# Optimization experiments

Hardware: AMD Instinct MI355X
Metric: run time of the kernel (lower is better)

Reference implementation:

```python
import jax, jax.numpy as jnp
import numpy as np

HID = 2048          # hidden_size
INTER = 4096        # expand * hidden_size
NH = 64             # num_heads
HD = 64             # head_dim (NH*HD == INTER)
N = 128             # ssm state_size
G = 1               # n_groups
K = 4               # conv_kernel
EPS = 1e-5
CONV_DIM = INTER + 2 * G * N            # 4352
PROJ = INTER + CONV_DIM + NH            # 8512 (d_mlp == 0)


def setup_inputs() -> dict:
    key = jax.random.key(0)
    ks = jax.random.split(key, 6)
    B, S = 2, 2048
    return {
        "hidden_states": jax.random.normal(ks[0], (B, S, HID), jnp.float32),
        "in_proj_w": jax.random.normal(ks[1], (PROJ, HID), jnp.float32) * 0.02,
        "conv_w": jax.random.normal(ks[2], (CONV_DIM, 1, K), jnp.float32) * 0.1,
        "conv_b": jax.random.normal(ks[3], (CONV_DIM,), jnp.float32) * 0.02,
        "dt_bias": jnp.ones((NH,), jnp.float32),
        "A_log": jnp.log(jnp.arange(1, NH + 1, dtype=jnp.float32)),
        "D": jnp.ones((NH,), jnp.float32),
        "norm_weight": jnp.ones((INTER,), jnp.float32),
        "out_proj_w": jax.random.normal(ks[4], (HID, INTER), jnp.float32) * 0.02,
    }


def _mamba2_forward(hidden_states, in_proj_w, conv_w, conv_b, dt_bias,
                    A_log, D, norm_weight, out_proj_w):
    b, sq, _ = hidden_states.shape
    # in_proj (d_mlp == 0, so split is gate | hidden_B_C | dt)
    proj = hidden_states @ in_proj_w.T                       # [b, s, PROJ]
    gate, hbc, dt = jnp.split(proj, [INTER, INTER + CONV_DIM], axis=-1)

    # causal depthwise conv1d over time + SiLU
    xc = jnp.transpose(hbc, (0, 2, 1))                       # [b, conv_dim, s]
    xc = jax.lax.conv_general_dilated(xc, conv_w, (1,), [(K - 1, 0)],
                                      feature_group_count=CONV_DIM)
    xc = xc + conv_b[None, :, None]
    hbc = jax.nn.silu(jnp.transpose(xc, (0, 2, 1)))          # [b, s, conv_dim]

    hs, Bm, Cm = jnp.split(hbc, [INTER, INTER + G * N], axis=-1)
    hs = hs.reshape(b, sq, NH, HD)
    Bm = jnp.repeat(Bm.reshape(b, sq, G, N), NH // G, axis=2)   # [b, s, nh, n]
    Cm = jnp.repeat(Cm.reshape(b, sq, G, N), NH // G, axis=2)

    A = -jnp.exp(A_log)                                      # [nh]
    dt = jax.nn.softplus(dt + dt_bias)                       # [b, s, nh]

    # selective SSM scan: state_t = exp(dt*A)*state_{t-1} + dt*B_t x_t^T
    def step(state, inp):
        xt, Bt, Ct, dtt = inp                                # [b,nh,hd],[b,nh,n],[b,nh,n],[b,nh]
        dA = jnp.exp(dtt * A)                                # [b, nh]
        state = state * dA[..., None, None] \
            + (dtt[..., None] * xt)[..., None] * Bt[:, :, None, :]
        y = jnp.einsum('bhdn,bhn->bhd', state, Ct)
        return state, y

    init = jnp.zeros((b, NH, HD, N), jnp.float32)
    xs = (jnp.moveaxis(hs, 1, 0), jnp.moveaxis(Bm, 1, 0),
          jnp.moveaxis(Cm, 1, 0), jnp.moveaxis(dt, 1, 0))
    _, ys = jax.lax.scan(step, init, xs)                     # [s, b, nh, hd]
    y = jnp.moveaxis(ys, 0, 1) + D[None, None, :, None] * hs
    y = y.reshape(b, sq, INTER)

    # gated RMSNorm (norm_before_gate=False): gate first, then normalize
    y = y * jax.nn.silu(gate)
    var = jnp.mean(y * y, axis=-1, keepdims=True)
    y = y * jax.lax.rsqrt(var + EPS) * norm_weight
    return y @ out_proj_w.T                                  # [b, s, HID]


def reference(hidden_states, in_proj_w, conv_w, conv_b, dt_bias, A_log, D,
              norm_weight, out_proj_w):
    return _mamba2_forward(hidden_states, in_proj_w, conv_w, conv_b, dt_bias,
                           A_log, D, norm_weight, out_proj_w)
```

## Files before the change

kernel.cpp:

```cpp
#include <hip/hip_runtime.h>
#include <hip/hip_bf16.h>
#include <cstddef>
#include <cstdint>

#define HID   2048
#define INTER 4096
#define NH    64
#define HD    64
#define NST   128
#define CONV_DIM 4352
#define PROJ  8512
#define PROJ_PAD 8704
#define SS    2048
#define BB    2
#define BS    (BB*SS)
#define EPS   1e-5f

#define COL_HS 4096
#define COL_B  8192
#define COL_C  8320
#define COL_DT 8448

#define NCH   16
#define CHUNK 128

#define CL    128
#define NCHK  16

typedef short s16x8 __attribute__((ext_vector_type(8)));
typedef float f32x4 __attribute__((ext_vector_type(4)));

__device__ inline ushort f2b(float x) {
  __hip_bfloat16 h = __float2bfloat16(x);
  return *(ushort*)&h;
}
__device__ inline float b2f(ushort u) {
  unsigned int v = ((unsigned int)u) << 16;
  return __uint_as_float(v);
}
__device__ inline int swz(int row, int e) { return row * 128 + (e ^ ((row & 7) << 3)); }

__device__ inline void gload16(const void* g, void* l) {
  __builtin_amdgcn_global_load_lds((const __attribute__((address_space(1))) void*)g,
                                   (__attribute__((address_space(3))) void*)l, 16, 0, 0);
}

__global__ __launch_bounds__(256) void to_bf16(const float* __restrict__ src,
                                               ushort* __restrict__ dst, long n4) {
  long i = (long)blockIdx.x * 256 + threadIdx.x;
  if (i >= n4) return;
  float4 v = *(const float4*)(src + i * 4);
  ushort4 o;
  o.x = f2b(v.x); o.y = f2b(v.y); o.z = f2b(v.z); o.w = f2b(v.w);
  *(ushort4*)(dst + i * 4) = o;
}

__global__ __launch_bounds__(256) void to_bf16_pad(const float* __restrict__ src,
                                                   ushort* __restrict__ dst, long n4) {
  long i = (long)blockIdx.x * 256 + threadIdx.x;
  if (i >= n4) return;
  long e0 = i * 4;
  long row = e0 >> 11;
  ushort4 o;
  if (row < PROJ) {
    float4 v = *(const float4*)(src + e0);
    o.x = f2b(v.x); o.y = f2b(v.y); o.z = f2b(v.z); o.w = f2b(v.w);
  } else {
    o.x = o.y = o.z = o.w = 0;
  }
  *(ushort4*)(dst + e0) = o;
}

__global__ __launch_bounds__(512, 2) void gemm256_8ph(
    const ushort* __restrict__ A, const ushort* __restrict__ Bw,
    float* __restrict__ C) {
  __shared__ ushort smem[65536];
  const int tid = threadIdx.x;
  const int lane = tid & 63;
  const int wid = tid >> 6;
  const int wm = wid >> 2;
  const int wn = wid & 3;
  const int r = lane & 15;
  const int kx = lane >> 4;

  const int fid = blockIdx.x;
  const int bcol = ((fid >> 7) << 3) + ((fid & 127) >> 4);
  const int brow = fid & 15;

  const ushort* Ag = A + (size_t)(brow * 256) * HID;
  const ushort* Bg = Bw + (size_t)(bcol * 256) * HID;

  const int srow = tid >> 3;
  const int scole = (((tid & 7) * 16) ^ ((srow & 7) << 4)) >> 1;

  auto stageA = [&](int buf, int kt, int half) {
    const ushort* g = Ag + (size_t)(half * 128 + srow) * HID + kt * 64 + scole;
    ushort* l = smem + buf * 16384 + half * 8192 + tid * 8;
    gload16(g, l);
    gload16(g + (size_t)64 * HID, l + 4096);
  };
  auto stageB = [&](int buf, int kt, int half) {
    const ushort* g = Bg + (size_t)(half * 128 + srow) * HID + kt * 64 + scole;
    ushort* l = smem + 32768 + buf * 16384 + half * 8192 + tid * 8;
    gload16(g, l);
    gload16(g + (size_t)64 * HID, l + 4096);
  };
  auto ldA = [&](int buf, int mf, int ks) -> s16x8 {
    int row = wm * 128 + mf * 16 + r;
    int cb = (ks * 64 + kx * 16) ^ ((row & 7) << 4);
    return *(const s16x8*)(smem + buf * 16384 + row * 64 + (cb >> 1));
  };
  auto ldB = [&](int buf, int nf, int ks) -> s16x8 {
    int row = wn * 64 + nf * 16 + r;
    int cb = (ks * 64 + kx * 16) ^ ((row & 7) << 4);
    return *(const s16x8*)(smem + 32768 + buf * 16384 + row * 64 + (cb >> 1));
  };

  f32x4 acc[8][4];
#pragma unroll
  for (int i = 0; i < 8; i++)
#pragma unroll
    for (int j = 0; j < 4; j++) acc[i][j] = (f32x4)0.f;

  constexpr int NT = HID / 64;

  stageA(0, 0, 0); stageA(0, 0, 1);
  stageB(0, 0, 0); stageB(0, 0, 1);
  stageA(1, 1, 0); stageA(1, 1, 1);
  asm volatile("s_waitcnt vmcnt(4)" ::: "memory");
  __builtin_amdgcn_s_barrier();

  int cur = 0;
  for (int t = 0; t < NT; t++) {
    s16x8 a[4][2], b[2][2], b2[2][2];
#pragma unroll
    for (int mf = 0; mf < 4; mf++)
#pragma unroll
      for (int ks = 0; ks < 2; ks++) a[mf][ks] = ldA(cur, mf, ks);
#pragma unroll
    for (int nf = 0; nf < 2; nf++)
#pragma unroll
      for (int ks = 0; ks < 2; ks++) b[nf][ks] = ldB(cur, nf, ks);
    if (t + 1 < NT) stageB(cur ^ 1, t + 1, 0);
    __builtin_amdgcn_s_barrier();
    asm volatile("s_waitcnt lgkmcnt(0)" ::: "memory");
    __builtin_amdgcn_sched_barrier(0);
    __builtin_amdgcn_s_setprio(1);
#pragma unroll
    for (int mf = 0; mf < 4; mf++)
#pragma unroll
      for (int nf = 0; nf < 2; nf++)
#pragma unroll
        for (int ks = 0; ks < 2; ks++)
          acc[mf][nf] = __builtin_amdgcn_mfma_f32_16x16x32_bf16(a[mf][ks], b[nf][ks], acc[mf][nf], 0, 0, 0);
    __builtin_amdgcn_s_setprio(0);
    __builtin_amdgcn_s_barrier();
#pragma unroll
    for (int nf = 0; nf < 2; nf++)
#pragma unroll
      for (int ks = 0; ks < 2; ks++) b2[nf][ks] = ldB(cur, nf + 2, ks);
    if (t + 1 < NT) stageB(cur ^ 1, t + 1, 1);
    __builtin_amdgcn_s_barrier();
    asm volatile("s_waitcnt lgkmcnt(0)" ::: "memory");
    __builtin_amdgcn_sched_barrier(0);
    __builtin_amdgcn_s_setprio(1);
#pragma unroll
    for (int mf = 0; mf < 4; mf++)
#pragma unroll
      for (int nf = 0; nf < 2; nf++)
#pragma unroll
        for (int ks = 0; ks < 2; ks++)
          acc[mf][nf + 2] = __builtin_amdgcn_mfma_f32_16x16x32_bf16(a[mf][ks], b2[nf][ks], acc[mf][nf + 2], 0, 0, 0);
    __builtin_amdgcn_s_setprio(0);
    __builtin_amdgcn_s_barrier();
#pragma unroll
    for (int mf = 0; mf < 4; mf++)
#pragma unroll
      for (int ks = 0; ks < 2; ks++) a[mf][ks] = ldA(cur, mf + 4, ks);
    __builtin_amdgcn_s_barrier();
    asm volatile("s_waitcnt lgkmcnt(0)" ::: "memory");
    __builtin_amdgcn_sched_barrier(0);
    __builtin_amdgcn_s_setprio(1);
#pragma unroll
    for (int mf = 0; mf < 4; mf++)
#pragma unroll
      for (int nf = 0; nf < 2; nf++)
#pragma unroll
        for (int ks = 0; ks < 2; ks++)
          acc[mf + 4][nf] = __builtin_amdgcn_mfma_f32_16x16x32_bf16(a[mf][ks], b[nf][ks], acc[mf + 4][nf], 0, 0, 0);
    __builtin_amdgcn_s_setprio(0);
    __builtin_amdgcn_s_barrier();
    if (t + 2 < NT) { stageA(cur, t + 2, 0); stageA(cur, t + 2, 1); }
    __builtin_amdgcn_s_setprio(1);
#pragma unroll
    for (int mf = 0; mf < 4; mf++)
#pragma unroll
      for (int nf = 0; nf < 2; nf++)
#pragma unroll
        for (int ks = 0; ks < 2; ks++)
          acc[mf + 4][nf + 2] = __builtin_amdgcn_mfma_f32_16x16x32_bf16(a[mf][ks], b2[nf][ks], acc[mf + 4][nf + 2], 0, 0, 0);
    __builtin_amdgcn_s_setprio(0);
    if (t + 2 < NT) {
      asm volatile("s_waitcnt vmcnt(4)" ::: "memory");
    } else {
      asm volatile("s_waitcnt vmcnt(0)" ::: "memory");
    }
    __builtin_amdgcn_s_barrier();
    cur ^= 1;
  }

  const int m0 = brow * 256 + wm * 128 + (lane >> 4) * 4;
  const int n0 = bcol * 256 + wn * 64 + r;
#pragma unroll
  for (int mf = 0; mf < 8; mf++) {
#pragma unroll
    for (int nf = 0; nf < 4; nf++) {
      int n = n0 + nf * 16;
      if (n >= PROJ) continue;
#pragma unroll
      for (int q = 0; q < 4; q++)
        C[(size_t)(m0 + mf * 16 + q) * PROJ + n] = acc[mf][nf][q];
    }
  }
}

template <bool GUARD_N>
__global__ __launch_bounds__(256) void gemm_bt16(
    const ushort* __restrict__ A, int lda,
    const ushort* __restrict__ Bw, int ldb,
    float* __restrict__ C, int ldc, int Kd, int Nmax) {
  __shared__ short smem[8192];
  const int tid = threadIdx.x;
  const int lane = tid & 63;
  const int wid = tid >> 6;
  const int wm = wid >> 1, wn = wid & 1;
  const int r = lane & 15;
  const int kx = lane >> 4;

  const int fid = blockIdx.y * gridDim.x + blockIdx.x;
  const int bcol = ((fid >> 8) << 3) | ((fid & 255) >> 5);
  const int brow = fid & 31;

  const ushort* Ab = A + (size_t)(brow * 128) * lda;
  const ushort* Bb = Bw + (size_t)(bcol * 128) * ldb;

  f32x4 acc[4][4];
#pragma unroll
  for (int i = 0; i < 4; i++)
#pragma unroll
    for (int j = 0; j < 4; j++) acc[i][j] = (f32x4)0.f;

  const int u0 = tid, u1 = 256 + tid;
  const int row0 = u0 >> 2, kc0 = (u0 & 3) * 8;
  const int row1 = u1 >> 2, kc1 = (u1 & 3) * 8;

  const s16x8* As8 = (const s16x8*)smem;
  const s16x8* Bs8 = (const s16x8*)(smem + 4096);

  for (int k0 = 0; k0 < Kd; k0 += 32) {
    __syncthreads();
    gload16(Ab + (size_t)row0 * lda + k0 + kc0, smem + u0 * 8);
    gload16(Ab + (size_t)row1 * lda + k0 + kc1, smem + u1 * 8);
    gload16(Bb + (size_t)row0 * ldb + k0 + kc0, smem + 4096 + u0 * 8);
    gload16(Bb + (size_t)row1 * ldb + k0 + kc1, smem + 4096 + u1 * 8);
    __syncthreads();
    s16x8 af[4], bw[4];
#pragma unroll
    for (int i = 0; i < 4; i++) af[i] = As8[(wm * 64 + i * 16 + r) * 4 + kx];
#pragma unroll
    for (int j = 0; j < 4; j++) bw[j] = Bs8[(wn * 64 + j * 16 + r) * 4 + kx];
#pragma unroll
    for (int i = 0; i < 4; i++)
#pragma unroll
      for (int j = 0; j < 4; j++)
        acc[i][j] = __builtin_amdgcn_mfma_f32_16x16x32_bf16(af[i], bw[j], acc[i][j], 0, 0, 0);
  }

  const int m0 = brow * 128 + wm * 64 + (lane >> 4) * 4;
  const int n0 = bcol * 128 + wn * 64 + (lane & 15);
#pragma unroll
  for (int i = 0; i < 4; i++) {
#pragma unroll
    for (int j = 0; j < 4; j++) {
      int n = n0 + j * 16;
      if (GUARD_N && n >= Nmax) continue;
#pragma unroll
      for (int q = 0; q < 4; q++) {
        C[(size_t)(m0 + i * 16 + q) * ldc + n] = acc[i][j][q];
      }
    }
  }
}

__global__ void conv_capture(const float* __restrict__ proj, float* __restrict__ side) {
  int idx = blockIdx.x * 256 + threadIdx.x;
  const int total = BB * CONV_DIM * NCH * 3;
  if (idx >= total) return;
  int c = idx % CONV_DIM;
  int t = idx / CONV_DIM;
  int j = t % 3; t /= 3;
  int chunk = t % NCH;
  int b = t / NCH;
  int s = chunk * CHUNK - 1 - j;
  float v = (s >= 0) ? proj[((size_t)b * SS + s) * PROJ + COL_HS + c] : 0.f;
  side[((size_t)(b * NCH + chunk) * 3 + j) * CONV_DIM + c] = v;
}

__global__ void conv_silu(float* __restrict__ proj, const float* __restrict__ side,
                          const float* __restrict__ cw, const float* __restrict__ cb) {
  int idx = blockIdx.x * 256 + threadIdx.x;
  const int total = BB * CONV_DIM * NCH;
  if (idx >= total) return;
  int c = idx % CONV_DIM;
  int t = idx / CONV_DIM;
  int chunk = t % NCH;
  int b = t / NCH;
  float w0 = cw[c * 4 + 0], w1 = cw[c * 4 + 1], w2 = cw[c * 4 + 2], w3 = cw[c * 4 + 3];
  float bias = cb[c];
  const float* sd = side + ((size_t)(b * NCH + chunk) * 3) * CONV_DIM;
  float xm1 = sd[c];
  float xm2 = sd[CONV_DIM + c];
  float xm3 = sd[2 * CONV_DIM + c];
  size_t p = ((size_t)b * SS + (size_t)chunk * CHUNK) * PROJ + COL_HS + c;
  for (int s = 0; s < CHUNK; s++) {
    float xin = proj[p];
    float o = w3 * xin + w2 * xm1 + w1 * xm2 + w0 * xm3 + bias;
    o = o / (1.f + __expf(-o));
    proj[p] = o;
    xm3 = xm2; xm2 = xm1; xm1 = xin;
    p += PROJ;
  }
}

__global__ __launch_bounds__(256) void ssd_chunk_state(
    const float* __restrict__ proj, const float* __restrict__ dt_bias,
    const float* __restrict__ A_log, ushort* __restrict__ states,
    float* __restrict__ cumbuf, float* __restrict__ dtvbuf) {
  const int bid = blockIdx.x;
  const int c = bid & 15;
  const int h = (bid >> 4) & 63;
  const int b = bid >> 10;
  const int tid = threadIdx.x;
  const int lane = tid & 63;
  const int wv = tid >> 6;
  __shared__ float sdtv[CL], scum[CL], sw[CL];
  __shared__ ushort sBt[128 * 128];
  __shared__ ushort sXw[64 * 128];
  const size_t row0 = (size_t)b * SS + (size_t)c * CL;
  const size_t bh = (size_t)(b * NH + h);

  const float Ah = -__expf(A_log[h]);
  if (tid < CL) {
    float z = proj[(row0 + tid) * PROJ + COL_DT + h] + dt_bias[h];
    float dtv = (z > 20.f) ? z : log1pf(__expf(z));
    sdtv[tid] = dtv;
    sw[tid] = dtv * Ah;
  }
  __syncthreads();
  for (int off = 1; off < CL; off <<= 1) {
    float v = 0.f;
    if (tid < CL) { v = sw[tid]; if (tid >= off) v += sw[tid - off]; }
    __syncthreads();
    if (tid < CL) sw[tid] = v;
    __syncthreads();
  }
  if (tid < CL) {
    scum[tid] = sw[tid];
    cumbuf[bh * SS + c * CL + tid] = sw[tid];
    dtvbuf[bh * SS + c * CL + tid] = sdtv[tid];
  }
  __syncthreads();
  const float cumL = scum[CL - 1];
  if (tid < CL) sw[tid] = __expf(cumL - scum[tid]) * sdtv[tid];
  __syncthreads();

  {
    const int t = tid >> 1, n0 = (tid & 1) * 64;
    const float* src = proj + (row0 + t) * PROJ + COL_B + n0;
#pragma unroll
    for (int j = 0; j < 64; j += 4) {
      float4 v = *(const float4*)(src + j);
      sBt[swz(n0 + j + 0, t)] = f2b(v.x);
      sBt[swz(n0 + j + 1, t)] = f2b(v.y);
      sBt[swz(n0 + j + 2, t)] = f2b(v.z);
      sBt[swz(n0 + j + 3, t)] = f2b(v.w);
    }
  }
  {
    const int d = tid & 63;
    const int t0 = (tid >> 6) * 32;
    for (int t = t0; t < t0 + 32; t++) {
      float x = proj[(row0 + t) * PROJ + COL_HS + h * 64 + d];
      sXw[swz(d, t)] = f2b(x * sw[t]);
    }
  }
  __syncthreads();

  const int r = lane & 15, kx = lane >> 4;
  f32x4 acc[2][4];
#pragma unroll
  for (int i = 0; i < 2; i++)
#pragma unroll
    for (int j = 0; j < 4; j++) acc[i][j] = (f32x4)0.f;
#pragma unroll
  for (int kk = 0; kk < 4; kk++) {
    s16x8 a[2], bo[4];
#pragma unroll
    for (int i = 0; i < 2; i++)
      a[i] = *(const s16x8*)&sBt[swz(wv * 32 + i * 16 + r, kk * 32 + kx * 8)];
#pragma unroll
    for (int j = 0; j < 4; j++)
      bo[j] = *(const s16x8*)&sXw[swz(j * 16 + r, kk * 32 + kx * 8)];
#pragma unroll
    for (int i = 0; i < 2; i++)
#pragma unroll
      for (int j = 0; j < 4; j++)
        acc[i][j] = __builtin_amdgcn_mfma_f32_16x16x32_bf16(a[i], bo[j], acc[i][j], 0, 0, 0);
  }
  ushort* dst = states + (size_t)bid * (128 * 64);
#pragma unroll
  for (int i = 0; i < 2; i++) {
#pragma unroll
    for (int j = 0; j < 4; j++) {
      int n = wv * 32 + i * 16 + (lane >> 4) * 4;
      int d = (lane & 15) + j * 16;
      ushort4 o;
      o.x = f2b(acc[i][j][0]);
      o.y = f2b(acc[i][j][1]);
      o.z = f2b(acc[i][j][2]);
      o.w = f2b(acc[i][j][3]);
      *(ushort4*)(dst + (size_t)d * 128 + n) = o;
    }
  }
}

__global__ __launch_bounds__(256) void ssd_state_scan(
    ushort* __restrict__ states, const float* __restrict__ cumbuf) {
  const int bh = blockIdx.x;
  const int tid = threadIdx.x;
  float run[32];
#pragma unroll
  for (int i = 0; i < 32; i++) run[i] = 0.f;
  for (int c = 0; c < NCHK; c++) {
    float dec = __expf(cumbuf[(size_t)bh * SS + c * CL + (CL - 1)]);
    ushort* p = states + ((size_t)bh * NCHK + c) * 8192 + tid * 32;
    s16x8 in[4];
#pragma unroll
    for (int v = 0; v < 4; v++) in[v] = *(const s16x8*)(p + v * 8);
    s16x8 out[4];
#pragma unroll
    for (int v = 0; v < 4; v++) {
#pragma unroll
      for (int e = 0; e < 8; e++) {
        int i = v * 8 + e;
        out[v][e] = (short)f2b(run[i]);
        run[i] = dec * run[i] + b2f((ushort)in[v][e]);
      }
    }
#pragma unroll
    for (int v = 0; v < 4; v++) *(s16x8*)(p + v * 8) = out[v];
  }
}

__global__ __launch_bounds__(256, 2) void ssd_chunk_out(
    float* __restrict__ proj, const ushort* __restrict__ states,
    const float* __restrict__ cumbuf, const float* __restrict__ dtvbuf,
    const float* __restrict__ Dp) {
  const int bid = blockIdx.x;
  const int c = bid & 15;
  const int h = (bid >> 4) & 63;
  const int b = bid >> 10;
  const int tid = threadIdx.x;
  const int lane = tid & 63;
  const int wv = tid >> 6;
  __shared__ ushort sC[128 * 128];
  __shared__ ushort sB[128 * 128];
  __shared__ ushort sX[64 * 128];
  const size_t row0 = (size_t)b * SS + (size_t)c * CL;
  const size_t bh = (size_t)(b * NH + h);
  const float* cumb = cumbuf + bh * SS + c * CL;
  const float* dtvb = dtvbuf + bh * SS + c * CL;
  const int r = lane & 15, kx = lane >> 4;

  float ct[2][4];
#pragma unroll
  for (int i = 0; i < 2; i++)
#pragma unroll
    for (int q = 0; q < 4; q++)
      ct[i][q] = cumb[wv * 32 + i * 16 + ((lane >> 4) << 2) + q];
  float cumt[8], dvt[8];
#pragma unroll
  for (int j = 0; j < 8; j++) {
    int tau = j * 16 + (lane & 15);
    cumt[j] = cumb[tau];
    dvt[j] = dtvb[tau];
  }
  const float eC = __expf(cumb[wv * 32 + (lane >> 1)]);

  {
    const int t = tid >> 1, n0 = (tid & 1) * 64;
    const float* srcC = proj + (row0 + t) * PROJ + COL_C + n0;
    const float* srcB = proj + (row0 + t) * PROJ + COL_B + n0;
#pragma unroll
    for (int j = 0; j < 64; j += 8) {
      float4 c0 = *(const float4*)(srcC + j);
      float4 c1 = *(const float4*)(srcC + j + 4);
      s16x8 u;
      u[0] = (short)f2b(c0.x); u[1] = (short)f2b(c0.y);
      u[2] = (short)f2b(c0.z); u[3] = (short)f2b(c0.w);
      u[4] = (short)f2b(c1.x); u[5] = (short)f2b(c1.y);
      u[6] = (short)f2b(c1.z); u[7] = (short)f2b(c1.w);
      *(s16x8*)&sC[swz(t, n0 + j)] = u;
      float4 b0 = *(const float4*)(srcB + j);
      float4 b1 = *(const float4*)(srcB + j + 4);
      s16x8 w;
      w[0] = (short)f2b(b0.x); w[1] = (short)f2b(b0.y);
      w[2] = (short)f2b(b0.z); w[3] = (short)f2b(b0.w);
      w[4] = (short)f2b(b1.x); w[5] = (short)f2b(b1.y);
      w[6] = (short)f2b(b1.z); w[7] = (short)f2b(b1.w);
      *(s16x8*)&sB[swz(t, n0 + j)] = w;
    }
  }
  {
    const int d = tid & 63;
    const int t0 = (tid >> 6) * 32;
    for (int t = t0; t < t0 + 32; t++)
      sX[swz(d, t)] = f2b(proj[(row0 + t) * PROJ + COL_HS + h * 64 + d]);
  }
  __syncthreads();

  f32x4 g[2][8];
#pragma unroll
  for (int i = 0; i < 2; i++)
#pragma unroll
    for (int j = 0; j < 8; j++) g[i][j] = (f32x4)0.f;
#pragma unroll
  for (int kk = 0; kk < 4; kk++) {
    s16x8 a[2], bo[8];
#pragma unroll
    for (int i = 0; i < 2; i++)
      a[i] = *(const s16x8*)&sC[swz(wv * 32 + i * 16 + r, kk * 32 + kx * 8)];
#pragma unroll
    for (int j = 0; j < 8; j++)
      bo[j] = *(const s16x8*)&sB[swz(j * 16 + r, kk * 32 + kx * 8)];
#pragma unroll
    for (int i = 0; i < 2; i++)
#pragma unroll
      for (int j = 0; j < 8; j++)
        g[i][j] = __builtin_amdgcn_mfma_f32_16x16x32_bf16(a[i], bo[j], g[i][j], 0, 0, 0);
  }

  s16x8 spf[4][4];
  {
    const ushort* sp = states + (size_t)bid * 8192;
#pragma unroll
    for (int kk = 0; kk < 4; kk++)
#pragma unroll
      for (int j = 0; j < 4; j++)
        spf[kk][j] = *(const s16x8*)(sp + (size_t)(j * 16 + r) * 128 + kk * 32 + kx * 8);
  }
  __syncthreads();

#pragma unroll
  for (int j = 0; j < 8; j++) {
    float cu = cumt[j], dv = dvt[j];
    int tau = j * 16 + (lane & 15);
#pragma unroll
    for (int i = 0; i < 2; i++) {
#pragma unroll
      for (int q = 0; q < 4; q++) {
        int t = wv * 32 + i * 16 + ((lane >> 4) << 2) + q;
        float val = (tau <= t) ? g[i][j][q] * __expf(ct[i][q] - cu) * dv : 0.f;
        sB[swz(t, tau)] = f2b(val);
      }
    }
  }
  {
    int t = wv * 32 + (lane >> 1);
    int n0 = (lane & 1) * 64;
#pragma unroll
    for (int j = 0; j < 64; j += 8) {
      s16x8 u = *(const s16x8*)&sC[swz(t, n0 + j)];
#pragma unroll
      for (int k = 0; k < 8; k++) u[k] = (short)f2b(b2f((ushort)u[k]) * eC);
      *(s16x8*)&sC[swz(t, n0 + j)] = u;
    }
  }
  __syncthreads();

  f32x4 y[2][4];
#pragma unroll
  for (int i = 0; i < 2; i++)
#pragma unroll
    for (int j = 0; j < 4; j++) y[i][j] = (f32x4)0.f;
#pragma unroll
  for (int kk = 0; kk < 4; kk++) {
    s16x8 a[2], bo[4];
#pragma unroll
    for (int i = 0; i < 2; i++)
      a[i] = *(const s16x8*)&sB[swz(wv * 32 + i * 16 + r, kk * 32 + kx * 8)];
#pragma unroll
    for (int j = 0; j < 4; j++)
      bo[j] = *(const s16x8*)&sX[swz(j * 16 + r, kk * 32 + kx * 8)];
#pragma unroll
    for (int i = 0; i < 2; i++)
#pragma unroll
      for (int j = 0; j < 4; j++)
        y[i][j] = __builtin_amdgcn_mfma_f32_16x16x32_bf16(a[i], bo[j], y[i][j], 0, 0, 0);
  }
#pragma unroll
  for (int kk = 0; kk < 4; kk++) {
    s16x8 a[2];
#pragma unroll
    for (int i = 0; i < 2; i++)
      a[i] = *(const s16x8*)&sC[swz(wv * 32 + i * 16 + r, kk * 32 + kx * 8)];
#pragma unroll
    for (int i = 0; i < 2; i++)
#pragma unroll
      for (int j = 0; j < 4; j++)
        y[i][j] = __builtin_amdgcn_mfma_f32_16x16x32_bf16(a[i], spf[kk][j], y[i][j], 0, 0, 0);
  }

  const float Dh = Dp[h];
#pragma unroll
  for (int i = 0; i < 2; i++) {
#pragma unroll
    for (int j = 0; j < 4; j++) {
      int t0 = wv * 32 + i * 16 + (lane >> 4) * 4;
      int d = (lane & 15) + j * 16;
#pragma unroll
      for (int q = 0; q < 4; q++) {
        float x = b2f(sX[swz(d, t0 + q)]);
        proj[(row0 + t0 + q) * PROJ + COL_HS + h * 64 + d] = y[i][j][q] + Dh * x;
      }
    }
  }
}

__global__ __launch_bounds__(256) void rmsnorm_kernel(
    const float* __restrict__ proj, const float* __restrict__ nw,
    ushort* __restrict__ y16) {
  const int row = blockIdx.x;
  const int tid = threadIdx.x;
  const float* yp = proj + (size_t)row * PROJ + COL_HS;
  const float* gp = proj + (size_t)row * PROJ;
  float v[16];
  float ss = 0.f;
#pragma unroll
  for (int q = 0; q < 4; q++) {
    int col = q * 1024 + tid * 4;
    float4 y = *(const float4*)(yp + col);
    float4 g = *(const float4*)(gp + col);
    float vy[4] = {y.x, y.y, y.z, y.w};
    float vg[4] = {g.x, g.y, g.z, g.w};
#pragma unroll
    for (int j = 0; j < 4; j++) {
      float sg = vg[j] / (1.f + __expf(-vg[j]));
      float vv = vy[j] * sg;
      v[q * 4 + j] = vv;
      ss += vv * vv;
    }
  }
#pragma unroll
  for (int o = 1; o < 64; o <<= 1) ss += __shfl_xor(ss, o);
  __shared__ float red[4];
  if ((tid & 63) == 0) red[tid >> 6] = ss;
  __syncthreads();
  float tot = red[0] + red[1] + red[2] + red[3];
  float scale = rsqrtf(tot * (1.f / INTER) + EPS);
#pragma unroll
  for (int q = 0; q < 4; q++) {
    int col = q * 1024 + tid * 4;
    float4 w = *(const float4*)(nw + col);
    ushort4 o;
    o.x = f2b(v[q * 4 + 0] * scale * w.x);
    o.y = f2b(v[q * 4 + 1] * scale * w.y);
    o.z = f2b(v[q * 4 + 2] * scale * w.z);
    o.w = f2b(v[q * 4 + 3] * scale * w.w);
    *(ushort4*)(y16 + (size_t)row * INTER + col) = o;
  }
}

extern "C" void kernel_launch(void* const* d_in, const int* in_sizes, int n_in,
                              void* d_out, int out_size, void* d_ws, size_t ws_size,
                              hipStream_t stream) {
  const float* hs   = (const float*)d_in[0];
  const float* w1   = (const float*)d_in[1];
  const float* cw   = (const float*)d_in[2];
  const float* cb   = (const float*)d_in[3];
  const float* dtb  = (const float*)d_in[4];
  const float* alog = (const float*)d_in[5];
  const float* Dp   = (const float*)d_in[6];
  const float* nw   = (const float*)d_in[7];
  const float* w2   = (const float*)d_in[8];
  float* out = (float*)d_out;

  char* base = (char*)d_ws;
  size_t off = 0;
  float* proj = (float*)(base + off); off += (size_t)BS * PROJ * 4;
  float* side = (float*)(base + off); off += (size_t)BB * NCH * 3 * CONV_DIM * 4;
  off = (off + 255) & ~(size_t)255;
  char* rC = base + off;
  ushort* hs16 = (ushort*)rC;
  ushort* w1p  = (ushort*)(rC + 16777216);
  ushort* states = (ushort*)rC;
  float*  cumbuf = (float*)(rC + 33554432);
  float*  dtvbuf = (float*)(rC + 33554432 + 1048576);
  ushort* w216 = (ushort*)rC;
  ushort* y16  = (ushort*)(rC + 16777216);

  {
    long n4 = (long)BS * HID / 4;
    to_bf16<<<(n4 + 255) / 256, 256, 0, stream>>>(hs, hs16, n4);
  }
  {
    long n4 = (long)PROJ_PAD * HID / 4;
    to_bf16_pad<<<(n4 + 255) / 256, 256, 0, stream>>>(w1, w1p, n4);
  }

  gemm256_8ph<<<(BS / 256) * (PROJ_PAD / 256), 512, 0, stream>>>(hs16, w1p, proj);

  conv_capture<<<(BB * CONV_DIM * NCH * 3 + 255) / 256, 256, 0, stream>>>(proj, side);
  conv_silu<<<(BB * CONV_DIM * NCH + 255) / 256, 256, 0, stream>>>(proj, side, cw, cb);

  ssd_chunk_state<<<BB * NH * NCHK, 256, 0, stream>>>(proj, dtb, alog, states, cumbuf, dtvbuf);
  ssd_state_scan<<<BB * NH, 256, 0, stream>>>(states, cumbuf);
  ssd_chunk_out<<<BB * NH * NCHK, 256, 0, stream>>>(proj, states, cumbuf, dtvbuf, Dp);

  {
    long n4 = (long)HID * INTER / 4;
    to_bf16<<<(n4 + 255) / 256, 256, 0, stream>>>(w2, w216, n4);
  }

  rmsnorm_kernel<<<BS, 256, 0, stream>>>(proj, nw, y16);

  gemm_bt16<false><<<dim3(HID / 128, BS / 128), 256, 0, stream>>>(
      y16, INTER, w216, INTER, out, HID, INTER, HID);
}
```

Before: 497.3 us.

## Store projection buffer in bf16 end-to-end and restage GEMM B prefetch

The in_proj GEMM now writes its output as bf16 instead of fp32, halving the intermediate buffer that conv, SSD and rmsnorm read and write. A separate fp32 copy of the dt columns is kept so the softplus input stays at full precision. Downstream kernels drop their fp32-to-bf16 conversions, and rmsnorm writes its normalized output in place, which the out_proj GEMM then reads with a strided lda. The GEMM's B-tile prefetch is also moved to issue two tiles ahead alongside A, with deeper vmcnt waits. The cost is lower precision on the conv and SSD inputs and outputs.

Result: faster. 478.0 us (-3.9%).

```diff
diff --git a/kernel.cpp b/kernel.cpp
--- a/kernel.cpp
+++ b/kernel.cpp
@@ -73,7 +73,7 @@
 
 __global__ __launch_bounds__(512, 2) void gemm256_8ph(
     const ushort* __restrict__ A, const ushort* __restrict__ Bw,
-    float* __restrict__ C) {
+    ushort* __restrict__ C, float* __restrict__ dtbuf) {
   __shared__ ushort smem[65536];
   const int tid = threadIdx.x;
   const int lane = tid & 63;
@@ -127,7 +127,8 @@
   stageA(0, 0, 0); stageA(0, 0, 1);
   stageB(0, 0, 0); stageB(0, 0, 1);
   stageA(1, 1, 0); stageA(1, 1, 1);
-  asm volatile("s_waitcnt vmcnt(4)" ::: "memory");
+  stageB(1, 1, 0); stageB(1, 1, 1);
+  asm volatile("s_waitcnt vmcnt(8)" ::: "memory");
   __builtin_amdgcn_s_barrier();
 
   int cur = 0;
@@ -141,7 +142,6 @@
     for (int nf = 0; nf < 2; nf++)
 #pragma unroll
       for (int ks = 0; ks < 2; ks++) b[nf][ks] = ldB(cur, nf, ks);
-    if (t + 1 < NT) stageB(cur ^ 1, t + 1, 0);
     __builtin_amdgcn_s_barrier();
     asm volatile("s_waitcnt lgkmcnt(0)" ::: "memory");
     __builtin_amdgcn_sched_barrier(0);
@@ -159,7 +159,6 @@
     for (int nf = 0; nf < 2; nf++)
 #pragma unroll
       for (int ks = 0; ks < 2; ks++) b2[nf][ks] = ldB(cur, nf + 2, ks);
-    if (t + 1 < NT) stageB(cur ^ 1, t + 1, 1);
     __builtin_amdgcn_s_barrier();
     asm volatile("s_waitcnt lgkmcnt(0)" ::: "memory");
     __builtin_amdgcn_sched_barrier(0);
@@ -190,7 +189,10 @@
           acc[mf + 4][nf] = __builtin_amdgcn_mfma_f32_16x16x32_bf16(a[mf][ks], b[nf][ks], acc[mf + 4][nf], 0, 0, 0);
     __builtin_amdgcn_s_setprio(0);
     __builtin_amdgcn_s_barrier();
-    if (t + 2 < NT) { stageA(cur, t + 2, 0); stageA(cur, t + 2, 1); }
+    if (t + 2 < NT) {
+      stageA(cur, t + 2, 0); stageA(cur, t + 2, 1);
+      stageB(cur, t + 2, 0); stageB(cur, t + 2, 1);
+    }
     __builtin_amdgcn_s_setprio(1);
 #pragma unroll
     for (int mf = 0; mf < 4; mf++)
@@ -201,7 +203,7 @@
           acc[mf + 4][nf + 2] = __builtin_amdgcn_mfma_f32_16x16x32_bf16(a[mf][ks], b2[nf][ks], acc[mf + 4][nf + 2], 0, 0, 0);
     __builtin_amdgcn_s_setprio(0);
     if (t + 2 < NT) {
-      asm volatile("s_waitcnt vmcnt(4)" ::: "memory");
+      asm volatile("s_waitcnt vmcnt(8)" ::: "memory");
     } else {
       asm volatile("s_waitcnt vmcnt(0)" ::: "memory");
     }
@@ -218,17 +220,20 @@
       int n = n0 + nf * 16;
       if (n >= PROJ) continue;
 #pragma unroll
-      for (int q = 0; q < 4; q++)
-        C[(size_t)(m0 + mf * 16 + q) * PROJ + n] = acc[mf][nf][q];
-    }
-  }
-}
-
-template <bool GUARD_N>
+      for (int q = 0; q < 4; q++) {
+        float v = acc[mf][nf][q];
+        int m = m0 + mf * 16 + q;
+        C[(size_t)m * PROJ + n] = f2b(v);
+        if (n >= COL_DT) dtbuf[(size_t)m * 64 + (n - COL_DT)] = v;
+      }
+    }
+  }
+}
+
 __global__ __launch_bounds__(256) void gemm_bt16(
     const ushort* __restrict__ A, int lda,
     const ushort* __restrict__ Bw, int ldb,
-    float* __restrict__ C, int ldc, int Kd, int Nmax) {
+    float* __restrict__ C, int ldc, int Kd) {
   __shared__ short smem[8192];
   const int tid = threadIdx.x;
   const int lane = tid & 63;
@@ -283,7 +288,6 @@
 #pragma unroll
     for (int j = 0; j < 4; j++) {
       int n = n0 + j * 16;
-      if (GUARD_N && n >= Nmax) continue;
 #pragma unroll
       for (int q = 0; q < 4; q++) {
         C[(size_t)(m0 + i * 16 + q) * ldc + n] = acc[i][j][q];
@@ -292,7 +296,7 @@
   }
 }
 
-__global__ void conv_capture(const float* __restrict__ proj, float* __restrict__ side) {
+__global__ void conv_capture(const ushort* __restrict__ proj, ushort* __restrict__ side) {
   int idx = blockIdx.x * 256 + threadIdx.x;
   const int total = BB * CONV_DIM * NCH * 3;
   if (idx >= total) return;
@@ -302,11 +306,11 @@
   int chunk = t % NCH;
   int b = t / NCH;
   int s = chunk * CHUNK - 1 - j;
-  float v = (s >= 0) ? proj[((size_t)b * SS + s) * PROJ + COL_HS + c] : 0.f;
+  ushort v = (s >= 0) ? proj[((size_t)b * SS + s) * PROJ + COL_HS + c] : (ushort)0;
   side[((size_t)(b * NCH + chunk) * 3 + j) * CONV_DIM + c] = v;
 }
 
-__global__ void conv_silu(float* __restrict__ proj, const float* __restrict__ side,
+__global__ void conv_silu(ushort* __restrict__ proj, const ushort* __restrict__ side,
                           const float* __restrict__ cw, const float* __restrict__ cb) {
   int idx = blockIdx.x * 256 + threadIdx.x;
   const int total = BB * CONV_DIM * NCH;
@@ -317,25 +321,26 @@
   int b = t / NCH;
   float w0 = cw[c * 4 + 0], w1 = cw[c * 4 + 1], w2 = cw[c * 4 + 2], w3 = cw[c * 4 + 3];
   float bias = cb[c];
-  const float* sd = side + ((size_t)(b * NCH + chunk) * 3) * CONV_DIM;
-  float xm1 = sd[c];
-  float xm2 = sd[CONV_DIM + c];
-  float xm3 = sd[2 * CONV_DIM + c];
+  const ushort* sd = side + ((size_t)(b * NCH + chunk) * 3) * CONV_DIM;
+  float xm1 = b2f(sd[c]);
+  float xm2 = b2f(sd[CONV_DIM + c]);
+  float xm3 = b2f(sd[2 * CONV_DIM + c]);
   size_t p = ((size_t)b * SS + (size_t)chunk * CHUNK) * PROJ + COL_HS + c;
   for (int s = 0; s < CHUNK; s++) {
-    float xin = proj[p];
+    float xin = b2f(proj[p]);
     float o = w3 * xin + w2 * xm1 + w1 * xm2 + w0 * xm3 + bias;
     o = o / (1.f + __expf(-o));
-    proj[p] = o;
+    proj[p] = f2b(o);
     xm3 = xm2; xm2 = xm1; xm1 = xin;
     p += PROJ;
   }
 }
 
 __global__ __launch_bounds__(256) void ssd_chunk_state(
-    const float* __restrict__ proj, const float* __restrict__ dt_bias,
-    const float* __restrict__ A_log, ushort* __restrict__ states,
-    float* __restrict__ cumbuf, float* __restrict__ dtvbuf) {
+    const ushort* __restrict__ proj, const float* __restrict__ dtf,
+    const float* __restrict__ dt_bias, const float* __restrict__ A_log,
+    ushort* __restrict__ states, float* __restrict__ cumbuf,
+    float* __restrict__ dtvbuf) {
   const int bid = blockIdx.x;
   const int c = bid & 15;
   const int h = (bid >> 4) & 63;
@@ -351,7 +356,7 @@
 
   const float Ah = -__expf(A_log[h]);
   if (tid < CL) {
-    float z = proj[(row0 + tid) * PROJ + COL_DT + h] + dt_bias[h];
+    float z = dtf[(row0 + tid) * 64 + h] + dt_bias[h];
     float dtv = (z > 20.f) ? z : log1pf(__expf(z));
     sdtv[tid] = dtv;
     sw[tid] = dtv * Ah;
@@ -376,21 +381,19 @@
 
   {
     const int t = tid >> 1, n0 = (tid & 1) * 64;
-    const float* src = proj + (row0 + t) * PROJ + COL_B + n0;
-#pragma unroll
-    for (int j = 0; j < 64; j += 4) {
-      float4 v = *(const float4*)(src + j);
-      sBt[swz(n0 + j + 0, t)] = f2b(v.x);
-      sBt[swz(n0 + j + 1, t)] = f2b(v.y);
-      sBt[swz(n0 + j + 2, t)] = f2b(v.z);
-      sBt[swz(n0 + j + 3, t)] = f2b(v.w);
+    const ushort* src = proj + (row0 + t) * PROJ + COL_B + n0;
+#pragma unroll
+    for (int j = 0; j < 64; j += 8) {
+      s16x8 v = *(const s16x8*)(src + j);
+#pragma unroll
+      for (int e = 0; e < 8; e++) sBt[swz(n0 + j + e, t)] = (ushort)v[e];
     }
   }
   {
     const int d = tid & 63;
     const int t0 = (tid >> 6) * 32;
     for (int t = t0; t < t0 + 32; t++) {
-      float x = proj[(row0 + t) * PROJ + COL_HS + h * 64 + d];
+      float x = b2f(proj[(row0 + t) * PROJ + COL_HS + h * 64 + d]);
       sXw[swz(d, t)] = f2b(x * sw[t]);
     }
   }
@@ -463,7 +466,7 @@
 }
 
 __global__ __launch_bounds__(256, 2) void ssd_chunk_out(
-    float* __restrict__ proj, const ushort* __restrict__ states,
+    ushort* __restrict__ proj, const ushort* __restrict__ states,
     const float* __restrict__ cumbuf, const float* __restrict__ dtvbuf,
     const float* __restrict__ Dp) {
   const int bid = blockIdx.x;
@@ -499,33 +502,19 @@
 
   {
     const int t = tid >> 1, n0 = (tid & 1) * 64;
-    const float* srcC = proj + (row0 + t) * PROJ + COL_C + n0;
-    const float* srcB = proj + (row0 + t) * PROJ + COL_B + n0;
+    const ushort* srcC = proj + (row0 + t) * PROJ + COL_C + n0;
+    const ushort* srcB = proj + (row0 + t) * PROJ + COL_B + n0;
 #pragma unroll
     for (int j = 0; j < 64; j += 8) {
-      float4 c0 = *(const float4*)(srcC + j);
-      float4 c1 = *(const float4*)(srcC + j + 4);
-      s16x8 u;
-      u[0] = (short)f2b(c0.x); u[1] = (short)f2b(c0.y);
-      u[2] = (short)f2b(c0.z); u[3] = (short)f2b(c0.w);
-      u[4] = (short)f2b(c1.x); u[5] = (short)f2b(c1.y);
-      u[6] = (short)f2b(c1.z); u[7] = (short)f2b(c1.w);
-      *(s16x8*)&sC[swz(t, n0 + j)] = u;
-      float4 b0 = *(const float4*)(srcB + j);
-      float4 b1 = *(const float4*)(srcB + j + 4);
-      s16x8 w;
-      w[0] = (short)f2b(b0.x); w[1] = (short)f2b(b0.y);
-      w[2] = (short)f2b(b0.z); w[3] = (short)f2b(b0.w);
-      w[4] = (short)f2b(b1.x); w[5] = (short)f2b(b1.y);
-      w[6] = (short)f2b(b1.z); w[7] = (short)f2b(b1.w);
-      *(s16x8*)&sB[swz(t, n0 + j)] = w;
+      *(s16x8*)&sC[swz(t, n0 + j)] = *(const s16x8*)(srcC + j);
+      *(s16x8*)&sB[swz(t, n0 + j)] = *(const s16x8*)(srcB + j);
     }
   }
   {
     const int d = tid & 63;
     const int t0 = (tid >> 6) * 32;
     for (int t = t0; t < t0 + 32; t++)
-      sX[swz(d, t)] = f2b(proj[(row0 + t) * PROJ + COL_HS + h * 64 + d]);
+      sX[swz(d, t)] = proj[(row0 + t) * PROJ + COL_HS + h * 64 + d];
   }
   __syncthreads();
 
@@ -631,28 +620,27 @@
 #pragma unroll
       for (int q = 0; q < 4; q++) {
         float x = b2f(sX[swz(d, t0 + q)]);
-        proj[(row0 + t0 + q) * PROJ + COL_HS + h * 64 + d] = y[i][j][q] + Dh * x;
+        proj[(row0 + t0 + q) * PROJ + COL_HS + h * 64 + d] = f2b(y[i][j][q] + Dh * x);
       }
     }
   }
 }
 
 __global__ __launch_bounds__(256) void rmsnorm_kernel(
-    const float* __restrict__ proj, const float* __restrict__ nw,
-    ushort* __restrict__ y16) {
+    ushort* __restrict__ proj, const float* __restrict__ nw) {
   const int row = blockIdx.x;
   const int tid = threadIdx.x;
-  const float* yp = proj + (size_t)row * PROJ + COL_HS;
-  const float* gp = proj + (size_t)row * PROJ;
+  ushort* yp = proj + (size_t)row * PROJ + COL_HS;
+  const ushort* gp = proj + (size_t)row * PROJ;
   float v[16];
   float ss = 0.f;
 #pragma unroll
   for (int q = 0; q < 4; q++) {
     int col = q * 1024 + tid * 4;
-    float4 y = *(const float4*)(yp + col);
-    float4 g = *(const float4*)(gp + col);
-    float vy[4] = {y.x, y.y, y.z, y.w};
-    float vg[4] = {g.x, g.y, g.z, g.w};
+    ushort4 yv = *(const ushort4*)(yp + col);
+    ushort4 gv = *(const ushort4*)(gp + col);
+    float vy[4] = {b2f(yv.x), b2f(yv.y), b2f(yv.z), b2f(yv.w)};
+    float vg[4] = {b2f(gv.x), b2f(gv.y), b2f(gv.z), b2f(gv.w)};
 #pragma unroll
     for (int j = 0; j < 4; j++) {
       float sg = vg[j] / (1.f + __expf(-vg[j]));
@@ -677,7 +665,7 @@
     o.y = f2b(v[q * 4 + 1] * scale * w.y);
     o.z = f2b(v[q * 4 + 2] * scale * w.z);
     o.w = f2b(v[q * 4 + 3] * scale * w.w);
-    *(ushort4*)(y16 + (size_t)row * INTER + col) = o;
+    *(ushort4*)(yp + col) = o;
   }
 }
 
@@ -697,8 +685,10 @@
 
   char* base = (char*)d_ws;
   size_t off = 0;
-  float* proj = (float*)(base + off); off += (size_t)BS * PROJ * 4;
-  float* side = (float*)(base + off); off += (size_t)BB * NCH * 3 * CONV_DIM * 4;
+  ushort* proj = (ushort*)(base + off); off += (size_t)BS * PROJ * 2;
+  ushort* side = (ushort*)(base + off); off += (size_t)BB * NCH * 3 * CONV_DIM * 2;
+  off = (off + 255) & ~(size_t)255;
+  float* dtbuf = (float*)(base + off); off += (size_t)BS * 64 * 4;
   off = (off + 255) & ~(size_t)255;
   char* rC = base + off;
   ushort* hs16 = (ushort*)rC;
@@ -707,7 +697,6 @@
   float*  cumbuf = (float*)(rC + 33554432);
   float*  dtvbuf = (float*)(rC + 33554432 + 1048576);
   ushort* w216 = (ushort*)rC;
-  ushort* y16  = (ushort*)(rC + 16777216);
 
   {
     long n4 = (long)BS * HID / 4;
@@ -718,12 +707,12 @@
     to_bf16_pad<<<(n4 + 255) / 256, 256, 0, stream>>>(w1, w1p, n4);
   }
 
-  gemm256_8ph<<<(BS / 256) * (PROJ_PAD / 256), 512, 0, stream>>>(hs16, w1p, proj);
+  gemm256_8ph<<<(BS / 256) * (PROJ_PAD / 256), 512, 0, stream>>>(hs16, w1p, proj, dtbuf);
 
   conv_capture<<<(BB * CONV_DIM * NCH * 3 + 255) / 256, 256, 0, stream>>>(proj, side);
   conv_silu<<<(BB * CONV_DIM * NCH + 255) / 256, 256, 0, stream>>>(proj, side, cw, cb);
 
-  ssd_chunk_state<<<BB * NH * NCHK, 256, 0, stream>>>(proj, dtb, alog, states, cumbuf, dtvbuf);
+  ssd_chunk_state<<<BB * NH * NCHK, 256, 0, stream>>>(proj, dtbuf, dtb, alog, states, cumbuf, dtvbuf);
   ssd_state_scan<<<BB * NH, 256, 0, stream>>>(states, cumbuf);
   ssd_chunk_out<<<BB * NH * NCHK, 256, 0, stream>>>(proj, states, cumbuf, dtvbuf, Dp);
 
@@ -732,8 +721,8 @@
     to_bf16<<<(n4 + 255) / 256, 256, 0, stream>>>(w2, w216, n4);
   }
 
-  rmsnorm_kernel<<<BS, 256, 0, stream>>>(proj, nw, y16);
-
-  gemm_bt16<false><<<dim3(HID / 128, BS / 128), 256, 0, stream>>>(
-      y16, INTER, w216, INTER, out, HID, INTER, HID);
-}
+  rmsnorm_kernel<<<BS, 256, 0, stream>>>(proj, nw);
+
+  gemm_bt16<<<dim3(HID / 128, BS / 128), 256, 0, stream>>>(
+      (const ushort*)(proj + COL_HS), PROJ, w216, INTER, out, HID, INTER);
+}
```
